# Kernel optimization log

Measured on AMD Instinct MI355X. Metric: run time of the kernel, lower is better.

## Reference

```python
import jax, jax.numpy as jnp
import numpy as np

BSZ, SEQ, DIM = 4, 4096, 1024
MEASURE_DIM = 64
TOPK = 16
NUM_TARGETS = 1


def fwht(x):
    """Fast Walsh-Hadamard transform over last dim (power of two), orthonormal scaling."""
    n = x.shape[-1]
    y = x
    h = 1
    while h < n:
        y = y.reshape(*y.shape[:-1], -1, 2, h)
        a, b = y[..., 0, :], y[..., 1, :]
        y = jnp.concatenate((a + b, a - b), axis=-1)
        y = y.reshape(*x.shape[:-1], n)
        h *= 2
    return y * (n ** -0.5)


def setup_inputs() -> dict:
    key = jax.random.key(0)
    kx, kg, ka, kt, ks, kp = jax.random.split(key, 6)
    x = jax.random.normal(kx, (BSZ, SEQ, DIM), dtype=jnp.float32)
    gates = jax.random.uniform(kg, (BSZ, NUM_TARGETS, MEASURE_DIM), dtype=jnp.float32) + 0.5
    alpha = jax.random.uniform(ka, (BSZ, NUM_TARGETS, 1), dtype=jnp.float32) * 0.1
    tau = jax.random.uniform(kt, (BSZ, NUM_TARGETS, 1), dtype=jnp.float32) * 0.02
    signs = jnp.where(jax.random.uniform(ks, (DIM,)) > 0.5, 1.0, -1.0).astype(jnp.float32)
    perm = jax.random.permutation(kp, DIM).astype(jnp.int32)
    inv_perm = jnp.argsort(perm).astype(jnp.int32)
    return {"x": x, "gates": gates, "alpha": alpha, "tau": tau,
            "signs": signs, "perm": perm, "inv_perm": inv_perm, "target_idx": 0}


def reference(x, gates, alpha, tau, signs, perm, inv_perm, target_idx):
    signs_ = signs.astype(x.dtype)
    # ---- sense: sign flip -> permute -> FWHT -> truncate ----
    y = jnp.take((x * signs_[None, None, :]), perm, axis=-1)
    z = fwht(y)[..., :MEASURE_DIM]  # [B, S, m]
    # ---- shrink (topk mode) ----
    gate = gates[:, target_idx][:, None, :]            # [B, 1, m]
    alpha_t = alpha[:, target_idx][:, None, :]         # [B, 1, 1]
    tau_t = jnp.abs(tau[:, target_idx])[:, None, :]    # [B, 1, 1]
    gated = gate * z
    agated = jnp.abs(gated)
    _, idx = jax.lax.top_k(agated, TOPK)               # [B, S, k]
    mask = jax.nn.one_hot(idx, MEASURE_DIM, dtype=gated.dtype).sum(-2)  # [B, S, m]
    sparse = jnp.where((mask > 0) & (agated >= tau_t), gated, jnp.zeros_like(gated))
    zs = alpha_t * sparse
    # ---- reconstruct: pad -> FWHT -> inverse permute -> sign flip ----
    full = jnp.zeros((*zs.shape[:-1], DIM), dtype=zs.dtype).at[..., :MEASURE_DIM].set(zs)
    r = jnp.take(fwht(full), inv_perm, axis=-1) * signs_[None, None, :]
    return x + r
```

## Files before the change

### kernel.cpp

```cpp
#include <hip/hip_runtime.h>

#define SEQ 4096
#define DIM 1024
#define MD 64
#define TOPK 16
#define WPB 2
#define RPW 2
#define RPB (WPB * RPW)

typedef float nfloat4 __attribute__((ext_vector_type(4)));

__global__ __launch_bounds__(WPB * 64) void csa_kernel(
    const float* __restrict__ x,
    const float* __restrict__ gates,
    const float* __restrict__ alpha,
    const float* __restrict__ tau,
    const float* __restrict__ signs,
    const int*   __restrict__ perm,
    const int*   __restrict__ inv_perm,
    const int*   __restrict__ target_idx,
    float*       __restrict__ out)
{
    __shared__ float y[RPB][DIM];

    const int lane = threadIdx.x & 63;
    const int wv   = threadIdx.x >> 6;
    const int r0   = (blockIdx.x * WPB + wv) * RPW;
    const int b    = r0 >> 12;

    float* y0 = y[wv * RPW + 0];
    float* y1 = y[wv * RPW + 1];

    #pragma unroll
    for (int c = 0; c < 4; ++c) {
        const float4 sg = ((const float4*)signs)[c * 64 + lane];
        const float4 xa = ((const float4*)(x + (size_t)(r0 + 0) * DIM))[c * 64 + lane];
        const float4 xb = ((const float4*)(x + (size_t)(r0 + 1) * DIM))[c * 64 + lane];
        float4 a, bq;
        a.x  = xa.x * sg.x; a.y  = xa.y * sg.y; a.z  = xa.z * sg.z; a.w  = xa.w * sg.w;
        bq.x = xb.x * sg.x; bq.y = xb.y * sg.y; bq.z = xb.z * sg.z; bq.w = xb.w * sg.w;
        ((float4*)y0)[c * 64 + lane] = a;
        ((float4*)y1)[c * 64 + lane] = bq;
    }

    int   pk[16];
    float ya[16], yb[16];
    float s0 = 0.f, s1 = 0.f;
    #pragma unroll
    for (int k = 0; k < 16; ++k) {
        pk[k] = perm[lane + 64 * k];
        ya[k] = y0[pk[k]];
        yb[k] = y1[pk[k]];
        s0 += ya[k];
        s1 += yb[k];
    }

    float v0 = s0, v1 = s1;
    #pragma unroll
    for (int bit = 1; bit < MD; bit <<= 1) {
        const float o0 = __shfl_xor(v0, bit, 64);
        const float o1 = __shfl_xor(v1, bit, 64);
        v0 = (lane & bit) ? (o0 - v0) : (v0 + o0);
        v1 = (lane & bit) ? (o1 - v1) : (v1 + o1);
    }

    const int   ti   = target_idx[0];
    const float gate = gates[(b + ti) * MD + lane];
    const float tauv = fabsf(tau[b + ti]);
    const float al   = alpha[b + ti];

    const float g0 = gate * v0 * 0.03125f;
    const float g1 = gate * v1 * 0.03125f;
    const float ag0 = fabsf(g0), ag1 = fabsf(g1);

    const unsigned ka0 = __float_as_uint(ag0);
    const unsigned ka1 = __float_as_uint(ag1);
    unsigned T0 = 0u, T1 = 0u;
    #pragma unroll
    for (int bit = 30; bit >= 0; --bit) {
        const unsigned c0 = T0 | (1u << bit);
        const unsigned c1 = T1 | (1u << bit);
        if (__popcll(__ballot(ka0 >= c0)) >= TOPK) T0 = c0;
        if (__popcll(__ballot(ka1 >= c1)) >= TOPK) T1 = c1;
    }
    const int ngt0 = __popcll(__ballot(ka0 > T0));
    const int ngt1 = __popcll(__ballot(ka1 > T1));
    const unsigned long long lm = (1ull << lane) - 1ull;
    const int er0 = __popcll(__ballot(ka0 == T0) & lm);
    const int er1 = __popcll(__ballot(ka1 == T1) & lm);
    const bool k0 = (ka0 > T0) || ((ka0 == T0) && (er0 < TOPK - ngt0));
    const bool k1 = (ka1 > T1) || ((ka1 == T1) && (er1 < TOPK - ngt1));

    float zs0 = (k0 && ag0 >= tauv) ? al * g0 : 0.f;
    float zs1 = (k1 && ag1 >= tauv) ? al * g1 : 0.f;

    #pragma unroll
    for (int bit = 1; bit < MD; bit <<= 1) {
        const float o0 = __shfl_xor(zs0, bit, 64);
        const float o1 = __shfl_xor(zs1, bit, 64);
        zs0 = (lane & bit) ? (o0 - zs0) : (zs0 + o0);
        zs1 = (lane & bit) ? (o1 - zs1) : (zs1 + o1);
    }
    const float w0 = zs0 * 0.03125f;
    const float w1 = zs1 * 0.03125f;

    #pragma unroll
    for (int k = 0; k < 16; ++k) {
        y0[pk[k]] = ya[k] + w0;
        y1[pk[k]] = yb[k] + w1;
    }

    nfloat4* out0 = (nfloat4*)(out + (size_t)(r0 + 0) * DIM);
    nfloat4* out1 = (nfloat4*)(out + (size_t)(r0 + 1) * DIM);
    #pragma unroll
    for (int c = 0; c < 4; ++c) {
        const float4 sg = ((const float4*)signs)[c * 64 + lane];
        const float4 t0 = ((const float4*)y0)[c * 64 + lane];
        const float4 t1 = ((const float4*)y1)[c * 64 + lane];
        nfloat4 o0, o1;
        o0.x = sg.x * t0.x; o0.y = sg.y * t0.y; o0.z = sg.z * t0.z; o0.w = sg.w * t0.w;
        o1.x = sg.x * t1.x; o1.y = sg.y * t1.y; o1.z = sg.z * t1.z; o1.w = sg.w * t1.w;
        __builtin_nontemporal_store(o0, &out0[c * 64 + lane]);
        __builtin_nontemporal_store(o1, &out1[c * 64 + lane]);
    }
}

extern "C" void kernel_launch(void* const* d_in, const int* in_sizes, int n_in,
                              void* d_out, int out_size, void* d_ws, size_t ws_size,
                              hipStream_t stream) {
    const float* x        = (const float*)d_in[0];
    const float* gates    = (const float*)d_in[1];
    const float* alpha    = (const float*)d_in[2];
    const float* tau      = (const float*)d_in[3];
    const float* signs    = (const float*)d_in[4];
    const int*   perm     = (const int*)d_in[5];
    const int*   inv_perm = (const int*)d_in[6];
    const int*   tgt      = (const int*)d_in[7];
    float*       out      = (float*)d_out;

    const int rows = 4 * SEQ;
    csa_kernel<<<rows / RPB, WPB * 64, 0, stream>>>(x, gates, alpha, tau, signs,
                                                    perm, inv_perm, tgt, out);
}
```

Before: 123.2 us.

## Compute output from x plus shuffled correction, drop LDS scatter, one row per wave

The output is computed directly as x + sign * w[inv_perm & 63]. The x row stays in registers, and each lane fetches the correction with a cross-lane shuffle indexed by inv_perm. This removes the second permuted LDS scatter and the LDS re-read before the store. Each wave now handles one row instead of two, with four waves per block, which gives more waves but less per-wave ILP. It also adds inv_perm loads and 16 shuffles per lane. x loads are now nontemporal.

```diff
diff --git a/kernel.cpp b/kernel.cpp
--- a/kernel.cpp
+++ b/kernel.cpp
@@ -4,9 +4,8 @@
 #define DIM 1024
 #define MD 64
 #define TOPK 16
-#define WPB 2
-#define RPW 2
-#define RPB (WPB * RPW)
+#define WPB 4
+#define RPB WPB
 
 typedef float nfloat4 __attribute__((ext_vector_type(4)));
 
@@ -25,43 +24,35 @@
 
     const int lane = threadIdx.x & 63;
     const int wv   = threadIdx.x >> 6;
-    const int r0   = (blockIdx.x * WPB + wv) * RPW;
-    const int b    = r0 >> 12;
+    const int r    = blockIdx.x * WPB + wv;
+    const int b    = r >> 12;
 
-    float* y0 = y[wv * RPW + 0];
-    float* y1 = y[wv * RPW + 1];
+    float* yr = y[wv];
+    const nfloat4* xrow = (const nfloat4*)(x + (size_t)r * DIM);
 
+    nfloat4 xs[4];
     #pragma unroll
     for (int c = 0; c < 4; ++c) {
+        xs[c] = __builtin_nontemporal_load(&xrow[c * 64 + lane]);
         const float4 sg = ((const float4*)signs)[c * 64 + lane];
-        const float4 xa = ((const float4*)(x + (size_t)(r0 + 0) * DIM))[c * 64 + lane];
-        const float4 xb = ((const float4*)(x + (size_t)(r0 + 1) * DIM))[c * 64 + lane];
-        float4 a, bq;
-        a.x  = xa.x * sg.x; a.y  = xa.y * sg.y; a.z  = xa.z * sg.z; a.w  = xa.w * sg.w;
-        bq.x = xb.x * sg.x; bq.y = xb.y * sg.y; bq.z = xb.z * sg.z; bq.w = xb.w * sg.w;
-        ((float4*)y0)[c * 64 + lane] = a;
-        ((float4*)y1)[c * 64 + lane] = bq;
+        float4 a;
+        a.x = xs[c].x * sg.x; a.y = xs[c].y * sg.y;
+        a.z = xs[c].z * sg.z; a.w = xs[c].w * sg.w;
+        ((float4*)yr)[c * 64 + lane] = a;
     }
 
-    int   pk[16];
-    float ya[16], yb[16];
-    float s0 = 0.f, s1 = 0.f;
+    float s = 0.f;
     #pragma unroll
     for (int k = 0; k < 16; ++k) {
-        pk[k] = perm[lane + 64 * k];
-        ya[k] = y0[pk[k]];
-        yb[k] = y1[pk[k]];
-        s0 += ya[k];
-        s1 += yb[k];
+        const int p = perm[lane + 64 * k];
+        s += yr[p];
     }
 
-    float v0 = s0, v1 = s1;
+    float v = s;
     #pragma unroll
     for (int bit = 1; bit < MD; bit <<= 1) {
-        const float o0 = __shfl_xor(v0, bit, 64);
-        const float o1 = __shfl_xor(v1, bit, 64);
-        v0 = (lane & bit) ? (o0 - v0) : (v0 + o0);
-        v1 = (lane & bit) ? (o1 - v1) : (v1 + o1);
+        const float o = __shfl_xor(v, bit, 64);
+        v = (lane & bit) ? (o - v) : (v + o);
     }
 
     const int   ti   = target_idx[0];
@@ -69,59 +60,45 @@
     const float tauv = fabsf(tau[b + ti]);
     const float al   = alpha[b + ti];
 
-    const float g0 = gate * v0 * 0.03125f;
-    const float g1 = gate * v1 * 0.03125f;
-    const float ag0 = fabsf(g0), ag1 = fabsf(g1);
+    const float g  = gate * v * 0.03125f;
+    const float ag = fabsf(g);
 
-    const unsigned ka0 = __float_as_uint(ag0);
-    const unsigned ka1 = __float_as_uint(ag1);
-    unsigned T0 = 0u, T1 = 0u;
+    const unsigned ka = __float_as_uint(ag);
+    unsigned T = 0u;
     #pragma unroll
     for (int bit = 30; bit >= 0; --bit) {
-        const unsigned c0 = T0 | (1u << bit);
-        const unsigned c1 = T1 | (1u << bit);
-        if (__popcll(__ballot(ka0 >= c0)) >= TOPK) T0 = c0;
-        if (__popcll(__ballot(ka1 >= c1)) >= TOPK) T1 = c1;
+        const unsigned cand = T | (1u << bit);
+        if (__popcll(__ballot(ka >= cand)) >= TOPK) T = cand;
     }
-    const int ngt0 = __popcll(__ballot(ka0 > T0));
-    const int ngt1 = __popcll(__ballot(ka1 > T1));
+    const int ngt = __popcll(__ballot(ka > T));
     const unsigned long long lm = (1ull << lane) - 1ull;
-    const int er0 = __popcll(__ballot(ka0 == T0) & lm);
-    const int er1 = __popcll(__ballot(ka1 == T1) & lm);
-    const bool k0 = (ka0 > T0) || ((ka0 == T0) && (er0 < TOPK - ngt0));
-    const bool k1 = (ka1 > T1) || ((ka1 == T1) && (er1 < TOPK - ngt1));
+    const int er = __popcll(__ballot(ka == T) & lm);
+    const bool keep = (ka > T) || ((ka == T) && (er < TOPK - ngt));
 
-    float zs0 = (k0 && ag0 >= tauv) ? al * g0 : 0.f;
-    float zs1 = (k1 && ag1 >= tauv) ? al * g1 : 0.f;
+    float zs = (keep && ag >= tauv) ? al * g : 0.f;
 
     #pragma unroll
     for (int bit = 1; bit < MD; bit <<= 1) {
-        const float o0 = __shfl_xor(zs0, bit, 64);
-        const float o1 = __shfl_xor(zs1, bit, 64);
-        zs0 = (lane & bit) ? (o0 - zs0) : (zs0 + o0);
-        zs1 = (lane & bit) ? (o1 - zs1) : (zs1 + o1);
+        const float o = __shfl_xor(zs, bit, 64);
+        zs = (lane & bit) ? (o - zs) : (zs + o);
     }
-    const float w0 = zs0 * 0.03125f;
-    const float w1 = zs1 * 0.03125f;
+    const float w = zs * 0.03125f;
 
-    #pragma unroll
-    for (int k = 0; k < 16; ++k) {
-        y0[pk[k]] = ya[k] + w0;
-        y1[pk[k]] = yb[k] + w1;
-    }
-
-    nfloat4* out0 = (nfloat4*)(out + (size_t)(r0 + 0) * DIM);
-    nfloat4* out1 = (nfloat4*)(out + (size_t)(r0 + 1) * DIM);
+    nfloat4* orow = (nfloat4*)(out + (size_t)r * DIM);
     #pragma unroll
     for (int c = 0; c < 4; ++c) {
+        const int4   ip = ((const int4*)inv_perm)[c * 64 + lane];
         const float4 sg = ((const float4*)signs)[c * 64 + lane];
-        const float4 t0 = ((const float4*)y0)[c * 64 + lane];
-        const float4 t1 = ((const float4*)y1)[c * 64 + lane];
-        nfloat4 o0, o1;
-        o0.x = sg.x * t0.x; o0.y = sg.y * t0.y; o0.z = sg.z * t0.z; o0.w = sg.w * t0.w;
-        o1.x = sg.x * t1.x; o1.y = sg.y * t1.y; o1.z = sg.z * t1.z; o1.w = sg.w * t1.w;
-        __builtin_nontemporal_store(o0, &out0[c * 64 + lane]);
-        __builtin_nontemporal_store(o1, &out1[c * 64 + lane]);
+        const float wx = __shfl(w, ip.x & 63, 64);
+        const float wy = __shfl(w, ip.y & 63, 64);
+        const float wz = __shfl(w, ip.z & 63, 64);
+        const float ww = __shfl(w, ip.w & 63, 64);
+        nfloat4 o;
+        o.x = xs[c].x + sg.x * wx;
+        o.y = xs[c].y + sg.y * wy;
+        o.z = xs[c].z + sg.z * wz;
+        o.w = xs[c].w + sg.w * ww;
+        __builtin_nontemporal_store(o, &orow[c * 64 + lane]);
     }
 }
 
```

New measurement: 133.4 us. 8.3% more time.

## Keep x rows in registers and apply reconstruction via inv_perm lane shuffles

Applied to the files above, without the earlier changes.

The output is now computed directly as x plus the sign-flipped reconstruction. The reconstruction value for each position is fetched with a lane shuffle indexed by inv_perm mod 64, replacing the scatter back into shared memory and the re-read. The x rows stay in registers across the kernel and are loaded with nontemporal hints. This removes the 16 scattered LDS writes and a full LDS row read per row, at the cost of more VGPRs and 32 shuffles per lane. It relies on the FWHT of a vector supported only on the first 64 entries being periodic mod 64.

```diff
diff --git a/kernel.cpp b/kernel.cpp
--- a/kernel.cpp
+++ b/kernel.cpp
@@ -30,29 +30,31 @@
 
     float* y0 = y[wv * RPW + 0];
     float* y1 = y[wv * RPW + 1];
+    const nfloat4* xrow0 = (const nfloat4*)(x + (size_t)(r0 + 0) * DIM);
+    const nfloat4* xrow1 = (const nfloat4*)(x + (size_t)(r0 + 1) * DIM);
 
+    nfloat4 xs0[4], xs1[4];
+    float4  sg[4];
     #pragma unroll
     for (int c = 0; c < 4; ++c) {
-        const float4 sg = ((const float4*)signs)[c * 64 + lane];
-        const float4 xa = ((const float4*)(x + (size_t)(r0 + 0) * DIM))[c * 64 + lane];
-        const float4 xb = ((const float4*)(x + (size_t)(r0 + 1) * DIM))[c * 64 + lane];
+        sg[c]  = ((const float4*)signs)[c * 64 + lane];
+        xs0[c] = __builtin_nontemporal_load(&xrow0[c * 64 + lane]);
+        xs1[c] = __builtin_nontemporal_load(&xrow1[c * 64 + lane]);
         float4 a, bq;
-        a.x  = xa.x * sg.x; a.y  = xa.y * sg.y; a.z  = xa.z * sg.z; a.w  = xa.w * sg.w;
-        bq.x = xb.x * sg.x; bq.y = xb.y * sg.y; bq.z = xb.z * sg.z; bq.w = xb.w * sg.w;
+        a.x  = xs0[c].x * sg[c].x; a.y  = xs0[c].y * sg[c].y;
+        a.z  = xs0[c].z * sg[c].z; a.w  = xs0[c].w * sg[c].w;
+        bq.x = xs1[c].x * sg[c].x; bq.y = xs1[c].y * sg[c].y;
+        bq.z = xs1[c].z * sg[c].z; bq.w = xs1[c].w * sg[c].w;
         ((float4*)y0)[c * 64 + lane] = a;
         ((float4*)y1)[c * 64 + lane] = bq;
     }
 
-    int   pk[16];
-    float ya[16], yb[16];
     float s0 = 0.f, s1 = 0.f;
     #pragma unroll
     for (int k = 0; k < 16; ++k) {
-        pk[k] = perm[lane + 64 * k];
-        ya[k] = y0[pk[k]];
-        yb[k] = y1[pk[k]];
-        s0 += ya[k];
-        s1 += yb[k];
+        const int p = perm[lane + 64 * k];
+        s0 += y0[p];
+        s1 += y1[p];
     }
 
     float v0 = s0, v1 = s1;
@@ -104,24 +106,30 @@
     const float w0 = zs0 * 0.03125f;
     const float w1 = zs1 * 0.03125f;
 
-    #pragma unroll
-    for (int k = 0; k < 16; ++k) {
-        y0[pk[k]] = ya[k] + w0;
-        y1[pk[k]] = yb[k] + w1;
-    }
-
-    nfloat4* out0 = (nfloat4*)(out + (size_t)(r0 + 0) * DIM);
-    nfloat4* out1 = (nfloat4*)(out + (size_t)(r0 + 1) * DIM);
+    nfloat4* orow0 = (nfloat4*)(out + (size_t)(r0 + 0) * DIM);
+    nfloat4* orow1 = (nfloat4*)(out + (size_t)(r0 + 1) * DIM);
     #pragma unroll
     for (int c = 0; c < 4; ++c) {
-        const float4 sg = ((const float4*)signs)[c * 64 + lane];
-        const float4 t0 = ((const float4*)y0)[c * 64 + lane];
-        const float4 t1 = ((const float4*)y1)[c * 64 + lane];
+        const int4 ip = ((const int4*)inv_perm)[c * 64 + lane];
+        const float wx0 = __shfl(w0, ip.x & 63, 64);
+        const float wy0 = __shfl(w0, ip.y & 63, 64);
+        const float wz0 = __shfl(w0, ip.z & 63, 64);
+        const float ww0 = __shfl(w0, ip.w & 63, 64);
+        const float wx1 = __shfl(w1, ip.x & 63, 64);
+        const float wy1 = __shfl(w1, ip.y & 63, 64);
+        const float wz1 = __shfl(w1, ip.z & 63, 64);
+        const float ww1 = __shfl(w1, ip.w & 63, 64);
         nfloat4 o0, o1;
-        o0.x = sg.x * t0.x; o0.y = sg.y * t0.y; o0.z = sg.z * t0.z; o0.w = sg.w * t0.w;
-        o1.x = sg.x * t1.x; o1.y = sg.y * t1.y; o1.z = sg.z * t1.z; o1.w = sg.w * t1.w;
-        __builtin_nontemporal_store(o0, &out0[c * 64 + lane]);
-        __builtin_nontemporal_store(o1, &out1[c * 64 + lane]);
+        o0.x = xs0[c].x + sg[c].x * wx0;
+        o0.y = xs0[c].y + sg[c].y * wy0;
+        o0.z = xs0[c].z + sg[c].z * wz0;
+        o0.w = xs0[c].w + sg[c].w * ww0;
+        o1.x = xs1[c].x + sg[c].x * wx1;
+        o1.y = xs1[c].y + sg[c].y * wy1;
+        o1.z = xs1[c].z + sg[c].z * wz1;
+        o1.w = xs1[c].w + sg[c].w * ww1;
+        __builtin_nontemporal_store(o0, &orow0[c * 64 + lane]);
+        __builtin_nontemporal_store(o1, &orow1[c * 64 + lane]);
     }
 }
 
```

Measured after the change: 129.2 us. 1.05x slower.

## Interleave four rows per wave in swizzled LDS and apply correction via shuffles

Applied to the files above, without the earlier changes.

Each wave now handles four rows. They are stored in LDS transposed as float4 per column index with an XOR swizzle, so one gather of a permuted index reads all four rows at once. The permuted scatter-back to LDS is replaced by reading inv_perm and fetching the per-column correction with a cross-lane shuffle from the owning lane. This cuts LDS gather and scatter traffic and bank conflicts, and amortises the butterfly and top-k ballots over more rows. The cost is higher register pressure and fewer blocks in the grid.

```diff
diff --git a/kernel.cpp b/kernel.cpp
--- a/kernel.cpp
+++ b/kernel.cpp
@@ -5,10 +5,12 @@
 #define MD 64
 #define TOPK 16
 #define WPB 2
-#define RPW 2
+#define RPW 4
 #define RPB (WPB * RPW)
 
 typedef float nfloat4 __attribute__((ext_vector_type(4)));
+
+__device__ __forceinline__ int swzU(int u) { return u ^ ((u >> 3) & 7); }
 
 __global__ __launch_bounds__(WPB * 64) void csa_kernel(
     const float* __restrict__ x,
@@ -21,47 +23,56 @@
     const int*   __restrict__ target_idx,
     float*       __restrict__ out)
 {
-    __shared__ float y[RPB][DIM];
+    __shared__ float lds[RPB * DIM];
 
     const int lane = threadIdx.x & 63;
     const int wv   = threadIdx.x >> 6;
     const int r0   = (blockIdx.x * WPB + wv) * RPW;
     const int b    = r0 >> 12;
 
-    float* y0 = y[wv * RPW + 0];
-    float* y1 = y[wv * RPW + 1];
+    float4* Lw = (float4*)(lds + wv * (RPW * DIM));
 
     #pragma unroll
     for (int c = 0; c < 4; ++c) {
         const float4 sg = ((const float4*)signs)[c * 64 + lane];
-        const float4 xa = ((const float4*)(x + (size_t)(r0 + 0) * DIM))[c * 64 + lane];
-        const float4 xb = ((const float4*)(x + (size_t)(r0 + 1) * DIM))[c * 64 + lane];
-        float4 a, bq;
-        a.x  = xa.x * sg.x; a.y  = xa.y * sg.y; a.z  = xa.z * sg.z; a.w  = xa.w * sg.w;
-        bq.x = xb.x * sg.x; bq.y = xb.y * sg.y; bq.z = xb.z * sg.z; bq.w = xb.w * sg.w;
-        ((float4*)y0)[c * 64 + lane] = a;
-        ((float4*)y1)[c * 64 + lane] = bq;
+        float4 a[RPW];
+        #pragma unroll
+        for (int r = 0; r < RPW; ++r) {
+            const float4 xv = ((const float4*)(x + (size_t)(r0 + r) * DIM))[c * 64 + lane];
+            a[r].x = xv.x * sg.x; a[r].y = xv.y * sg.y;
+            a[r].z = xv.z * sg.z; a[r].w = xv.w * sg.w;
+        }
+        const int d0 = c * 256 + 4 * lane;
+        float4 u0, u1, u2, u3;
+        u0.x = a[0].x; u0.y = a[1].x; u0.z = a[2].x; u0.w = a[3].x;
+        u1.x = a[0].y; u1.y = a[1].y; u1.z = a[2].y; u1.w = a[3].y;
+        u2.x = a[0].z; u2.y = a[1].z; u2.z = a[2].z; u2.w = a[3].z;
+        u3.x = a[0].w; u3.y = a[1].w; u3.z = a[2].w; u3.w = a[3].w;
+        Lw[swzU(d0 + 0)] = u0;
+        Lw[swzU(d0 + 1)] = u1;
+        Lw[swzU(d0 + 2)] = u2;
+        Lw[swzU(d0 + 3)] = u3;
     }
 
-    int   pk[16];
-    float ya[16], yb[16];
-    float s0 = 0.f, s1 = 0.f;
+    float s0 = 0.f, s1 = 0.f, s2 = 0.f, s3 = 0.f;
     #pragma unroll
     for (int k = 0; k < 16; ++k) {
-        pk[k] = perm[lane + 64 * k];
-        ya[k] = y0[pk[k]];
-        yb[k] = y1[pk[k]];
-        s0 += ya[k];
-        s1 += yb[k];
+        const int p = perm[lane + 64 * k];
+        const float4 q = Lw[swzU(p)];
+        s0 += q.x; s1 += q.y; s2 += q.z; s3 += q.w;
     }
 
-    float v0 = s0, v1 = s1;
+    float v0 = s0, v1 = s1, v2 = s2, v3 = s3;
     #pragma unroll
     for (int bit = 1; bit < MD; bit <<= 1) {
         const float o0 = __shfl_xor(v0, bit, 64);
         const float o1 = __shfl_xor(v1, bit, 64);
+        const float o2 = __shfl_xor(v2, bit, 64);
+        const float o3 = __shfl_xor(v3, bit, 64);
         v0 = (lane & bit) ? (o0 - v0) : (v0 + o0);
         v1 = (lane & bit) ? (o1 - v1) : (v1 + o1);
+        v2 = (lane & bit) ? (o2 - v2) : (v2 + o2);
+        v3 = (lane & bit) ? (o3 - v3) : (v3 + o3);
     }
 
     const int   ti   = target_idx[0];
@@ -71,57 +82,94 @@
 
     const float g0 = gate * v0 * 0.03125f;
     const float g1 = gate * v1 * 0.03125f;
-    const float ag0 = fabsf(g0), ag1 = fabsf(g1);
+    const float g2 = gate * v2 * 0.03125f;
+    const float g3 = gate * v3 * 0.03125f;
+    const float ag0 = fabsf(g0), ag1 = fabsf(g1), ag2 = fabsf(g2), ag3 = fabsf(g3);
 
     const unsigned ka0 = __float_as_uint(ag0);
     const unsigned ka1 = __float_as_uint(ag1);
-    unsigned T0 = 0u, T1 = 0u;
+    const unsigned ka2 = __float_as_uint(ag2);
+    const unsigned ka3 = __float_as_uint(ag3);
+    unsigned T0 = 0u, T1 = 0u, T2 = 0u, T3 = 0u;
     #pragma unroll
     for (int bit = 30; bit >= 0; --bit) {
         const unsigned c0 = T0 | (1u << bit);
         const unsigned c1 = T1 | (1u << bit);
+        const unsigned c2 = T2 | (1u << bit);
+        const unsigned c3 = T3 | (1u << bit);
         if (__popcll(__ballot(ka0 >= c0)) >= TOPK) T0 = c0;
         if (__popcll(__ballot(ka1 >= c1)) >= TOPK) T1 = c1;
+        if (__popcll(__ballot(ka2 >= c2)) >= TOPK) T2 = c2;
+        if (__popcll(__ballot(ka3 >= c3)) >= TOPK) T3 = c3;
     }
+    const unsigned long long lm = (1ull << lane) - 1ull;
     const int ngt0 = __popcll(__ballot(ka0 > T0));
     const int ngt1 = __popcll(__ballot(ka1 > T1));
-    const unsigned long long lm = (1ull << lane) - 1ull;
+    const int ngt2 = __popcll(__ballot(ka2 > T2));
+    const int ngt3 = __popcll(__ballot(ka3 > T3));
     const int er0 = __popcll(__ballot(ka0 == T0) & lm);
     const int er1 = __popcll(__ballot(ka1 == T1) & lm);
+    const int er2 = __popcll(__ballot(ka2 == T2) & lm);
+    const int er3 = __popcll(__ballot(ka3 == T3) & lm);
     const bool k0 = (ka0 > T0) || ((ka0 == T0) && (er0 < TOPK - ngt0));
     const bool k1 = (ka1 > T1) || ((ka1 == T1) && (er1 < TOPK - ngt1));
+    const bool k2 = (ka2 > T2) || ((ka2 == T2) && (er2 < TOPK - ngt2));
+    const bool k3 = (ka3 > T3) || ((ka3 == T3) && (er3 < TOPK - ngt3));
 
     float zs0 = (k0 && ag0 >= tauv) ? al * g0 : 0.f;
     float zs1 = (k1 && ag1 >= tauv) ? al * g1 : 0.f;
+    float zs2 = (k2 && ag2 >= tauv) ? al * g2 : 0.f;
+    float zs3 = (k3 && ag3 >= tauv) ? al * g3 : 0.f;
 
     #pragma unroll
     for (int bit = 1; bit < MD; bit <<= 1) {
         const float o0 = __shfl_xor(zs0, bit, 64);
         const float o1 = __shfl_xor(zs1, bit, 64);
+        const float o2 = __shfl_xor(zs2, bit, 64);
+        const float o3 = __shfl_xor(zs3, bit, 64);
         zs0 = (lane & bit) ? (o0 - zs0) : (zs0 + o0);
         zs1 = (lane & bit) ? (o1 - zs1) : (zs1 + o1);
+        zs2 = (lane & bit) ? (o2 - zs2) : (zs2 + o2);
+        zs3 = (lane & bit) ? (o3 - zs3) : (zs3 + o3);
     }
     const float w0 = zs0 * 0.03125f;
     const float w1 = zs1 * 0.03125f;
+    const float w2 = zs2 * 0.03125f;
+    const float w3 = zs3 * 0.03125f;
 
     #pragma unroll
-    for (int k = 0; k < 16; ++k) {
-        y0[pk[k]] = ya[k] + w0;
-        y1[pk[k]] = yb[k] + w1;
-    }
+    for (int c = 0; c < 4; ++c) {
+        const int4   ip = ((const int4*)inv_perm)[c * 64 + lane];
+        const float4 sg = ((const float4*)signs)[c * 64 + lane];
+        const int d0 = c * 256 + 4 * lane;
+        const float4 t0 = Lw[swzU(d0 + 0)];
+        const float4 t1 = Lw[swzU(d0 + 1)];
+        const float4 t2 = Lw[swzU(d0 + 2)];
+        const float4 t3 = Lw[swzU(d0 + 3)];
+        const int b0 = ip.x & 63, b1 = ip.y & 63, b2 = ip.z & 63, b3 = ip.w & 63;
 
-    nfloat4* out0 = (nfloat4*)(out + (size_t)(r0 + 0) * DIM);
-    nfloat4* out1 = (nfloat4*)(out + (size_t)(r0 + 1) * DIM);
-    #pragma unroll
-    for (int c = 0; c < 4; ++c) {
-        const float4 sg = ((const float4*)signs)[c * 64 + lane];
-        const float4 t0 = ((const float4*)y0)[c * 64 + lane];
-        const float4 t1 = ((const float4*)y1)[c * 64 + lane];
-        nfloat4 o0, o1;
-        o0.x = sg.x * t0.x; o0.y = sg.y * t0.y; o0.z = sg.z * t0.z; o0.w = sg.w * t0.w;
-        o1.x = sg.x * t1.x; o1.y = sg.y * t1.y; o1.z = sg.z * t1.z; o1.w = sg.w * t1.w;
-        __builtin_nontemporal_store(o0, &out0[c * 64 + lane]);
-        __builtin_nontemporal_store(o1, &out1[c * 64 + lane]);
+        nfloat4 o0, o1, o2, o3;
+        o0.x = sg.x * (t0.x + __shfl(w0, b0, 64));
+        o0.y = sg.y * (t1.x + __shfl(w0, b1, 64));
+        o0.z = sg.z * (t2.x + __shfl(w0, b2, 64));
+        o0.w = sg.w * (t3.x + __shfl(w0, b3, 64));
+        o1.x = sg.x * (t0.y + __shfl(w1, b0, 64));
+        o1.y = sg.y * (t1.y + __shfl(w1, b1, 64));
+        o1.z = sg.z * (t2.y + __shfl(w1, b2, 64));
+        o1.w = sg.w * (t3.y + __shfl(w1, b3, 64));
+        o2.x = sg.x * (t0.z + __shfl(w2, b0, 64));
+        o2.y = sg.y * (t1.z + __shfl(w2, b1, 64));
+        o2.z = sg.z * (t2.z + __shfl(w2, b2, 64));
+        o2.w = sg.w * (t3.z + __shfl(w2, b3, 64));
+        o3.x = sg.x * (t0.w + __shfl(w3, b0, 64));
+        o3.y = sg.y * (t1.w + __shfl(w3, b1, 64));
+        o3.z = sg.z * (t2.w + __shfl(w3, b2, 64));
+        o3.w = sg.w * (t3.w + __shfl(w3, b3, 64));
+
+        __builtin_nontemporal_store(o0, &((nfloat4*)(out + (size_t)(r0 + 0) * DIM))[c * 64 + lane]);
+        __builtin_nontemporal_store(o1, &((nfloat4*)(out + (size_t)(r0 + 1) * DIM))[c * 64 + lane]);
+        __builtin_nontemporal_store(o2, &((nfloat4*)(out + (size_t)(r0 + 2) * DIM))[c * 64 + lane]);
+        __builtin_nontemporal_store(o3, &((nfloat4*)(out + (size_t)(r0 + 3) * DIM))[c * 64 + lane]);
     }
 }
 
```

Measured after the change: 126.8 us. 1.03x slower.
